# Optimization experiments

Measured on AMD Instinct MI355X. Metric: run time of the kernel, lower is better.

The kernel has to match this reference:

```python
import jax, jax.numpy as jnp
import numpy as np

B, N, D = 8, 512, 512          # batch, seq_len, n_units (== d_in for residual)
H = 8                          # n_heads
DH = D // H                    # head dim
POS_CLIP = 60
EPS = 1e-7


def setup_inputs() -> dict:
    key = jax.random.key(0)
    ks = jax.random.split(key, 16)
    s = 0.02
    inp = {
        "query": jax.random.normal(ks[0], (B, N, D), dtype=jnp.float32),
        "valid_len": jax.random.randint(ks[1], (B,), 256, N + 1, dtype=jnp.int32),
        "Wq": jax.random.normal(ks[2], (D, D), dtype=jnp.float32) * s,
        "bq": jnp.zeros((D,), jnp.float32),
        "Wk": jax.random.normal(ks[3], (D, D), dtype=jnp.float32) * s,
        "bk": jnp.zeros((D,), jnp.float32),
        "Wv": jax.random.normal(ks[4], (D, D), dtype=jnp.float32) * s,
        "bv": jnp.zeros((D,), jnp.float32),
        "Wh": jax.random.normal(ks[5], (D, D), dtype=jnp.float32) * s,
        "bh": jnp.zeros((D,), jnp.float32),
        "pos_k": jax.random.uniform(ks[6], (2 * POS_CLIP + 1, DH), dtype=jnp.float32, minval=-0.05, maxval=0.05),
        "conv1_w": jax.random.normal(ks[7], (5, 5, H, 2 * H), dtype=jnp.float32) * s,  # HWIO
        "conv1_b": jnp.zeros((2 * H,), jnp.float32),
        "norm1_gamma": jnp.ones((2 * H,), jnp.float32),
        "norm1_beta": jnp.zeros((2 * H,), jnp.float32),
        "conv2_w": jax.random.normal(ks[8], (5, 5, 2 * H, H), dtype=jnp.float32) * s,
        "conv2_b": jnp.zeros((H,), jnp.float32),
        "ln_gamma": jnp.ones((D,), jnp.float32),
        "ln_beta": jnp.zeros((D,), jnp.float32),
    }
    return inp


def _conv_same(x, k, b):
    # x: [b, n, n, cin], k: [kh, kw, cin, cout] -> [b, n, n, cout]
    y = jax.lax.conv_general_dilated(x, k, window_strides=(1, 1), padding="SAME",
                                     dimension_numbers=("NHWC", "HWIO", "NHWC"))
    return y + b


def _norm_masked(x, valid_len, gamma, beta):
    # Norm(axes=[1,2]) with tf.nn.weighted_moments; mask over the query axis (axis 1).
    b, n, m, c = x.shape
    w = (jnp.arange(n)[None, :] < valid_len[:, None]).astype(x.dtype)  # [b, n]
    w4 = w[:, :, None, None]
    sw = valid_len.astype(x.dtype)[:, None, None, None] * m            # sum of broadcast weights
    mean = jnp.sum(w4 * x, axis=(1, 2), keepdims=True) / sw
    var = jnp.sum(w4 * (x - mean) ** 2, axis=(1, 2), keepdims=True) / sw
    return gamma * (x - mean) * jax.lax.rsqrt(var + EPS) + beta


def reference(query, valid_len, Wq, bq, Wk, bk, Wv, bv, Wh, bh, pos_k,
              conv1_w, conv1_b, norm1_gamma, norm1_beta, conv2_w, conv2_b,
              ln_gamma, ln_beta):
    b, n, d_in = query.shape
    # relative position indices (Shaw et al.), clipped to +/- POS_CLIP
    rel = jnp.clip(jnp.arange(n)[None, :] - jnp.arange(n)[:, None], -POS_CLIP, POS_CLIP) + POS_CLIP
    pos_enc = pos_k[rel]                                   # [n, n, dh]

    def heads(x):
        # tf.concat(tf.split(x, H, -1), 0): head-major blocks of size b
        return x.reshape(b, n, H, DH).transpose(2, 0, 1, 3)  # [h, b, n, dh]

    q = heads(query @ Wq + bq)
    k = heads(query @ Wk + bk)
    v = heads(query @ Wv + bv)

    scores = jnp.einsum("hbnd,hbmd->hbnm", q, k) + jnp.einsum("hbnd,nmd->hbnm", q, pos_enc)
    scores = scores / jnp.sqrt(jnp.asarray(DH, scores.dtype))

    # SelfCNN over attention maps: [b, n, n, h]
    maps = scores.transpose(1, 2, 3, 0)
    y = _conv_same(maps, conv1_w, conv1_b)
    y = _norm_masked(y, valid_len, norm1_gamma, norm1_beta)
    y = jax.nn.relu(y)
    y = _conv_same(y, conv2_w, conv2_b)                    # [b, n, n, h]
    scores = y.transpose(3, 0, 1, 2)                       # [h, b, n, m]

    seq_mask = jnp.arange(n)[None, :] < valid_len[:, None]  # [b, n] over key axis
    scores = jnp.where(seq_mask[None, :, None, :], scores, jnp.asarray(-1e12, scores.dtype))
    attn = jax.nn.softmax(scores, axis=-1)

    out = jnp.einsum("hbnm,hbmd->hbnd", attn, v)
    out = out.transpose(1, 2, 0, 3).reshape(b, n, H * DH)  # merge heads back
    out = out @ Wh + bh + query                            # residual

    mean = jnp.mean(out, axis=-1, keepdims=True)
    var = jnp.var(out, axis=-1, keepdims=True)
    return ln_gamma * (out - mean) * jax.lax.rsqrt(var + EPS) + ln_beta
```

## Files before the change

kernel.cpp:

```cpp
#include <hip/hip_runtime.h>

#define PC_ 60

typedef unsigned short u16;
typedef __attribute__((ext_vector_type(8))) short short8v;
typedef __attribute__((ext_vector_type(4))) float f32x4;

__device__ inline float bf2f(u16 u) {
    union { unsigned int i; float f; } x; x.i = ((unsigned)u) << 16; return x.f;
}
__device__ inline u16 f2bf(float f) {
    union { float f; unsigned int i; } x; x.f = f;
    unsigned int r = x.i + 0x7fff + ((x.i >> 16) & 1);
    return (u16)(r >> 16);
}
__device__ inline unsigned pk2(float a, float b) {
    return (unsigned)f2bf(a) | ((unsigned)f2bf(b) << 16);
}

__global__ __launch_bounds__(256) void k_prept(
    const float* __restrict__ W0, const float* __restrict__ W1,
    const float* __restrict__ W2, const float* __restrict__ W3,
    u16* __restrict__ T0, u16* __restrict__ T1, u16* __restrict__ T2, u16* __restrict__ T3,
    const float* __restrict__ c1w, const float* __restrict__ c2w,
    const float* __restrict__ pos_k,
    u16* __restrict__ Wf1, u16* __restrict__ Wf2, u16* __restrict__ pos_kb,
    const float* __restrict__ X, u16* __restrict__ Xb)
{
    const int z = blockIdx.z;
    const int t = threadIdx.x;
    if (z == 5) {
        const int blk = blockIdx.y * 8 + blockIdx.x;
#pragma unroll
        for (int k2 = 0; k2 < 16; ++k2) {
            const int i = ((blk * 16 + k2) * 256 + t) * 8;
            float4 a = *reinterpret_cast<const float4*>(X + i);
            float4 b = *reinterpret_cast<const float4*>(X + i + 4);
            *reinterpret_cast<uint4*>(Xb + i) =
                make_uint4(pk2(a.x, a.y), pk2(a.z, a.w), pk2(b.x, b.y), pk2(b.z, b.w));
        }
        return;
    }
    if (z == 4) {
        if (blockIdx.x != 0 || blockIdx.y != 0) return;
        for (int s = t; s < 448; s += 256) {
            const int q = s >> 6, l = s & 63, lg = l >> 4, n = l & 15;
            const int G = q * 4 + lg;
            unsigned o[4];
#pragma unroll
            for (int u2 = 0; u2 < 4; ++u2) {
                float v0 = 0.f, v1 = 0.f;
                if (G < 25) {
                    const int dn = G / 5, dm = G - dn * 5;
                    v0 = c1w[((dn * 5 + dm) * 8 + u2 * 2 + 0) * 16 + n];
                    v1 = c1w[((dn * 5 + dm) * 8 + u2 * 2 + 1) * 16 + n];
                }
                o[u2] = pk2(v0, v1);
            }
            *reinterpret_cast<uint4*>(&Wf1[s * 8]) = make_uint4(o[0], o[1], o[2], o[3]);
        }
        for (int s = t; s < 832; s += 256) {
            const int q = s >> 6, l = s & 63, lg = l >> 4, n = l & 15;
            const int G = q * 4 + lg;
            unsigned o[4];
#pragma unroll
            for (int u2 = 0; u2 < 4; ++u2) {
                float v0 = 0.f, v1 = 0.f;
                if (G < 50 && n < 8) {
                    const int pos = G >> 1, h = G & 1;
                    const int dn = pos / 5, dm = pos - dn * 5;
                    v0 = c2w[((dn * 5 + dm) * 16 + h * 8 + u2 * 2 + 0) * 8 + n];
                    v1 = c2w[((dn * 5 + dm) * 16 + h * 8 + u2 * 2 + 1) * 8 + n];
                }
                o[u2] = pk2(v0, v1);
            }
            *reinterpret_cast<uint4*>(&Wf2[s * 8]) = make_uint4(o[0], o[1], o[2], o[3]);
        }
        for (int s = t; s < 128 * 64; s += 256) {
            const int r = s >> 6;
            pos_kb[s] = (r < 121) ? f2bf(pos_k[s]) : (u16)0;
        }
        return;
    }
    const float* W = (z == 0) ? W0 : (z == 1) ? W1 : (z == 2) ? W2 : W3;
    u16* T        = (z == 0) ? T0 : (z == 1) ? T1 : (z == 2) ? T2 : T3;
    __shared__ float ls[64 * 65];
    const int k0 = blockIdx.x * 64, n0 = blockIdx.y * 64;
#pragma unroll
    for (int i = 0; i < 16; ++i) {
        const int idx = t + i * 256, r = idx >> 6, c = idx & 63;
        ls[c * 65 + r] = W[(size_t)(k0 + r) * 512 + n0 + c];
    }
    __syncthreads();
#pragma unroll
    for (int i = 0; i < 16; ++i) {
        const int idx = t + i * 256, r = idx >> 6, c = idx & 63;
        T[(size_t)(n0 + r) * 512 + k0 + c] = f2bf(ls[r * 65 + c]);
    }
}

__global__ __launch_bounds__(256) void k_qkvm(
    const u16* __restrict__ Xb,
    const u16* __restrict__ WT0, const u16* __restrict__ WT1, const u16* __restrict__ WT2,
    const float* __restrict__ b0, const float* __restrict__ b1, const float* __restrict__ b2,
    u16* __restrict__ Qb, u16* __restrict__ Kb, u16* __restrict__ Vt)
{
    const int z = blockIdx.z;
    const u16* WT    = (z == 0) ? WT0 : (z == 1) ? WT1 : WT2;
    const float* bias = (z == 0) ? b0 : (z == 1) ? b1 : b2;
    __shared__ __align__(16) u16 sh[18432];
    u16* As = sh; u16* Bs = sh + 9216;
    const int t = threadIdx.x, lane = t & 63, wave = t >> 6;
    const int wm = wave >> 1, wn = wave & 1;
    const int lg = lane >> 4, ln16 = lane & 15;
    const int m0 = blockIdx.x * 128, n0 = blockIdx.y * 128;
    f32x4 acc[4][4] = {};
    for (int k0 = 0; k0 < 512; k0 += 64) {
#pragma unroll
        for (int u = 0; u < 4; ++u) {
            const int chunk = u * 256 + t, row = chunk >> 3, ko = (chunk & 7) * 8;
            *reinterpret_cast<uint4*>(As + row * 72 + ko) =
                *reinterpret_cast<const uint4*>(Xb + (size_t)(m0 + row) * 512 + k0 + ko);
            *reinterpret_cast<uint4*>(Bs + row * 72 + ko) =
                *reinterpret_cast<const uint4*>(WT + (size_t)(n0 + row) * 512 + k0 + ko);
        }
        __syncthreads();
#pragma unroll
        for (int kk = 0; kk < 64; kk += 32) {
            short8v a[4], bfr[4];
#pragma unroll
            for (int mi = 0; mi < 4; ++mi)
                a[mi] = *reinterpret_cast<const short8v*>(As + (wm * 64 + mi * 16 + ln16) * 72 + kk + lg * 8);
#pragma unroll
            for (int ni = 0; ni < 4; ++ni)
                bfr[ni] = *reinterpret_cast<const short8v*>(Bs + (wn * 64 + ni * 16 + ln16) * 72 + kk + lg * 8);
#pragma unroll
            for (int mi = 0; mi < 4; ++mi)
#pragma unroll
                for (int ni = 0; ni < 4; ++ni)
                    acc[mi][ni] = __builtin_amdgcn_mfma_f32_16x16x32_bf16(a[mi], bfr[ni], acc[mi][ni], 0, 0, 0);
        }
        __syncthreads();
    }
    u16* Cs = sh + wave * 4608;
#pragma unroll
    for (int ni = 0; ni < 4; ++ni) {
        const float bv = bias[n0 + wn * 64 + ni * 16 + ln16];
#pragma unroll
        for (int mi = 0; mi < 4; ++mi)
#pragma unroll
            for (int r = 0; r < 4; ++r)
                Cs[(mi * 16 + lg * 4 + r) * 72 + ni * 16 + ln16] = f2bf(acc[mi][ni][r] + bv);
    }
    if (z < 2) {
        u16* O = (z == 0) ? Qb : Kb;
#pragma unroll
        for (int j = 0; j < 8; ++j) {
            const int chunk = j * 64 + lane, row = chunk >> 3, co = (chunk & 7) * 8;
            const int tok = m0 + wm * 64 + row;
            const int b = tok >> 9, n = tok & 511;
            const int cg = n0 + wn * 64 + co;
            const int h = cg >> 6, dh = cg & 63;
            *reinterpret_cast<uint4*>(O + ((size_t)((b * 8 + h) * 512 + n)) * 64 + dh) =
                *reinterpret_cast<const uint4*>(Cs + row * 72 + co);
        }
    } else {
#pragma unroll
        for (int j = 0; j < 8; ++j) {
            const int chunk = j * 64 + lane, dr = chunk >> 3, no8 = (chunk & 7) * 8;
            const int cg = n0 + wn * 64 + dr;
            const int h = cg >> 6, dh = cg & 63;
            const int tok = m0 + wm * 64 + no8;
            const int b = tok >> 9, n = tok & 511;
            u16 v[8];
#pragma unroll
            for (int e = 0; e < 8; ++e) v[e] = Cs[(no8 + e) * 72 + dr];
            uint4 o = make_uint4((unsigned)v[0] | ((unsigned)v[1] << 16),
                                 (unsigned)v[2] | ((unsigned)v[3] << 16),
                                 (unsigned)v[4] | ((unsigned)v[5] << 16),
                                 (unsigned)v[6] | ((unsigned)v[7] << 16));
            *reinterpret_cast<uint4*>(Vt + ((size_t)((b * 8 + h) * 64 + dh)) * 512 + n) = o;
        }
    }
}

__global__ __launch_bounds__(256) void k_qposm(
    const u16* __restrict__ Qb, const u16* __restrict__ pos_kb, u16* __restrict__ QP)
{
    __shared__ __align__(16) u16 sh[18432];
    u16* As = sh; u16* Bs = sh + 9216;
    const int t = threadIdx.x, lane = t & 63, wave = t >> 6;
    const int lg = lane >> 4, ln16 = lane & 15;
    const int n0 = blockIdx.x * 128, bh = blockIdx.y;
#pragma unroll
    for (int u = 0; u < 4; ++u) {
        const int chunk = u * 256 + t, row = chunk >> 3, ko = (chunk & 7) * 8;
        *reinterpret_cast<uint4*>(As + row * 72 + ko) =
            *reinterpret_cast<const uint4*>(Qb + ((size_t)(bh * 512 + n0 + row)) * 64 + ko);
        *reinterpret_cast<uint4*>(Bs + row * 72 + ko) =
            *reinterpret_cast<const uint4*>(pos_kb + (size_t)row * 64 + ko);
    }
    __syncthreads();
    f32x4 acc[2][8] = {};
#pragma unroll
    for (int kk = 0; kk < 64; kk += 32) {
        short8v a[2], bfr[8];
#pragma unroll
        for (int mi = 0; mi < 2; ++mi)
            a[mi] = *reinterpret_cast<const short8v*>(As + (wave * 32 + mi * 16 + ln16) * 72 + kk + lg * 8);
#pragma unroll
        for (int ni = 0; ni < 8; ++ni)
            bfr[ni] = *reinterpret_cast<const short8v*>(Bs + (ni * 16 + ln16) * 72 + kk + lg * 8);
#pragma unroll
        for (int mi = 0; mi < 2; ++mi)
#pragma unroll
            for (int ni = 0; ni < 8; ++ni)
                acc[mi][ni] = __builtin_amdgcn_mfma_f32_16x16x32_bf16(a[mi], bfr[ni], acc[mi][ni], 0, 0, 0);
    }
    __syncthreads();
    u16* Cs = sh + wave * 4352;
#pragma unroll
    for (int mi = 0; mi < 2; ++mi)
#pragma unroll
        for (int ni = 0; ni < 8; ++ni)
#pragma unroll
            for (int r = 0; r < 4; ++r)
                Cs[(mi * 16 + lg * 4 + r) * 136 + ni * 16 + ln16] = f2bf(acc[mi][ni][r]);
#pragma unroll
    for (int j = 0; j < 8; ++j) {
        const int chunk = j * 64 + lane, row = chunk >> 4, co = (chunk & 15) * 8;
        *reinterpret_cast<uint4*>(QP + ((size_t)(bh * 512 + n0 + wave * 32 + row)) * 128 + co) =
            *reinterpret_cast<const uint4*>(Cs + row * 136 + co);
    }
}

__global__ __launch_bounds__(256) void k_scoresm(
    const u16* __restrict__ Qb, const u16* __restrict__ Kb, const u16* __restrict__ QP,
    u16* __restrict__ S)
{
    __shared__ __align__(16) u16 sh[18432];
    u16* As = sh; u16* Bs = sh + 9216;
    const int t = threadIdx.x, lane = t & 63, wave = t >> 6;
    const int wm = wave >> 1, wn = wave & 1;
    const int lg = lane >> 4, ln16 = lane & 15;
    const int bid = blockIdx.x;
    const int bb = bid & 7;
    const int rest = bid >> 3;
    const int h = rest & 7;
    const int tile = rest >> 3;
    const int mx = tile & 3, my = tile >> 2;
    const int bh = bb * 8 + h;
    const int m0 = mx * 128, n0 = my * 128;
#pragma unroll
    for (int u = 0; u < 4; ++u) {
        const int chunk = u * 256 + t, row = chunk >> 3, ko = (chunk & 7) * 8;
        *reinterpret_cast<uint4*>(As + row * 72 + ko) =
            *reinterpret_cast<const uint4*>(Qb + ((size_t)(bh * 512 + n0 + row)) * 64 + ko);
        *reinterpret_cast<uint4*>(Bs + row * 72 + ko) =
            *reinterpret_cast<const uint4*>(Kb + ((size_t)(bh * 512 + m0 + row)) * 64 + ko);
    }
    __syncthreads();
    f32x4 acc[4][4] = {};
#pragma unroll
    for (int kk = 0; kk < 64; kk += 32) {
        short8v a[4], bfr[4];
#pragma unroll
        for (int mi = 0; mi < 4; ++mi)
            a[mi] = *reinterpret_cast<const short8v*>(As + (wm * 64 + mi * 16 + ln16) * 72 + kk + lg * 8);
#pragma unroll
        for (int ni = 0; ni < 4; ++ni)
            bfr[ni] = *reinterpret_cast<const short8v*>(Bs + (wn * 64 + ni * 16 + ln16) * 72 + kk + lg * 8);
#pragma unroll
        for (int mi = 0; mi < 4; ++mi)
#pragma unroll
            for (int ni = 0; ni < 4; ++ni)
                acc[mi][ni] = __builtin_amdgcn_mfma_f32_16x16x32_bf16(a[mi], bfr[ni], acc[mi][ni], 0, 0, 0);
    }
    __syncthreads();
    u16* QPs = sh;
#pragma unroll
    for (int u = 0; u < 8; ++u) {
        const int chunk = u * 256 + t, row = chunk >> 4, co = (chunk & 15) * 8;
        *reinterpret_cast<uint4*>(QPs + row * 128 + co) =
            *reinterpret_cast<const uint4*>(QP + ((size_t)(bh * 512 + n0 + row)) * 128 + co);
    }
    __syncthreads();
#pragma unroll
    for (int mi = 0; mi < 4; ++mi)
#pragma unroll
        for (int ni = 0; ni < 4; ++ni) {
            const int m_g = m0 + wn * 64 + ni * 16 + ln16;
#pragma unroll
            for (int r = 0; r < 4; ++r) {
                const int n_loc = wm * 64 + mi * 16 + lg * 4 + r;
                const int n_g = n0 + n_loc;
                int rel = m_g - n_g;
                rel = rel < -PC_ ? -PC_ : (rel > PC_ ? PC_ : rel);
                const float v = (acc[mi][ni][r] + bf2f(QPs[n_loc * 128 + rel + PC_])) * 0.125f;
                S[(size_t)bh * 262144 + (size_t)n_g * 512 + m_g] = f2bf(v);
            }
        }
}

__global__ __launch_bounds__(256) void k_conv1m(
    const u16* __restrict__ S, const u16* __restrict__ Wf,
    const float* __restrict__ bias, u16* __restrict__ Y,
    const int* __restrict__ VL, float* __restrict__ ST)
{
    __shared__ __align__(16) u16 xs[10368];
    __shared__ float wred[4][4][8];
    const int t = threadIdx.x;
    const int bid = blockIdx.x;
    const int b = bid & 7;
    const int rest = bid >> 3;
    const int m0 = (rest & 15) * 32;
    const int n0 = (rest >> 4) * 32;
    const u16* sp0 = S + (size_t)(b * 8) * 262144;
    for (int p = t; p < 648; p += 256) {
        const int idx2 = p * 2;
        const int r = idx2 / 36, c = idx2 - r * 36;
        const int gn = n0 - 2 + r, gm = m0 - 2 + c;
        uint4 o0 = make_uint4(0, 0, 0, 0), o1 = o0;
        if ((unsigned)gn < 512u && (unsigned)gm < 512u) {
            const u16* pp = sp0 + (size_t)gn * 512 + gm;
            unsigned u[8];
#pragma unroll
            for (int e = 0; e < 8; ++e)
                u[e] = *reinterpret_cast<const unsigned*>(pp + (size_t)e * 262144);
            o0 = make_uint4((u[0] & 0xffffu) | ((u[1] & 0xffffu) << 16),
                            (u[2] & 0xffffu) | ((u[3] & 0xffffu) << 16),
                            (u[4] & 0xffffu) | ((u[5] & 0xffffu) << 16),
                            (u[6] & 0xffffu) | ((u[7] & 0xffffu) << 16));
            o1 = make_uint4((u[0] >> 16) | (u[1] & 0xffff0000u),
                            (u[2] >> 16) | (u[3] & 0xffff0000u),
                            (u[4] >> 16) | (u[5] & 0xffff0000u),
                            (u[6] >> 16) | (u[7] & 0xffff0000u));
        }
        *reinterpret_cast<uint4*>(&xs[idx2 * 8]) = o0;
        *reinterpret_cast<uint4*>(&xs[(idx2 + 1) * 8]) = o1;
    }
    const int lane = t & 63, wave = t >> 6;
    const int lg = lane >> 4, ln16 = lane & 15;
    short8v bq[7];
#pragma unroll
    for (int q = 0; q < 7; ++q)
        bq[q] = *reinterpret_cast<const short8v*>(&Wf[(q * 64 + lane) * 8]);
    int aoff[7];
#pragma unroll
    for (int q = 0; q < 7; ++q) {
        const int G = q * 4 + lg; const int p = (G < 25) ? G : 0;
        const int dn = p / 5, dm = p - dn * 5;
        aoff[q] = (dn * 36 + dm) * 8;
    }
    const float4 b4 = *reinterpret_cast<const float4*>(&bias[lg * 4]);
    const int vl = VL[b];
    f32x4 sstv = {0.f, 0.f, 0.f, 0.f}, sst2v = {0.f, 0.f, 0.f, 0.f};
    __syncthreads();
    for (int i = 0; i < 16; ++i) {
        const int j = wave * 16 + i;
        const int tr = j >> 1, c0 = (j & 1) << 4;
        const int pb = (tr * 36 + c0 + ln16) * 8;
        f32x4 acc = {b4.x, b4.y, b4.z, b4.w};
#pragma unroll
        for (int q = 0; q < 7; ++q) {
            short8v a = *reinterpret_cast<const short8v*>(&xs[pb + aoff[q]]);
            acc = __builtin_amdgcn_mfma_f32_16x16x32_bf16(bq[q], a, acc, 0, 0, 0);
        }
        u16* yb = Y + (((size_t)(b * 512 + n0 + tr)) * 512 + (m0 + c0 + ln16)) * 16 + lg * 4;
        *reinterpret_cast<uint2*>(yb) = make_uint2(pk2(acc[0], acc[1]), pk2(acc[2], acc[3]));
        if (n0 + tr < vl) {
            sstv += acc;
            sst2v += acc * acc;
        }
    }
#pragma unroll
    for (int o = 1; o < 16; o <<= 1) {
#pragma unroll
        for (int r = 0; r < 4; ++r) {
            sstv[r]  += __shfl_xor(sstv[r], o);
            sst2v[r] += __shfl_xor(sst2v[r], o);
        }
    }
    if (ln16 == 0) {
#pragma unroll
        for (int r = 0; r < 4; ++r) {
            wred[wave][lg][r]     = sstv[r];
            wred[wave][lg][4 + r] = sst2v[r];
        }
    }
    __syncthreads();
    if (t < 16) {
        const int lgg = t >> 2, r = t & 3;
        const float a  = wred[0][lgg][r] + wred[1][lgg][r] + wred[2][lgg][r] + wred[3][lgg][r];
        const float b2 = wred[0][lgg][4 + r] + wred[1][lgg][4 + r] + wred[2][lgg][4 + r] + wred[3][lgg][4 + r];
        atomicAdd(&ST[(b * 16 + t) * 2 + 0], a);
        atomicAdd(&ST[(b * 16 + t) * 2 + 1], b2);
    }
}

__global__ __launch_bounds__(256) void k_conv2m(
    const u16* __restrict__ Y, const float* __restrict__ ST,
    const int* __restrict__ VL, const float* __restrict__ n1g, const float* __restrict__ n1b,
    const u16* __restrict__ Wf, const float* __restrict__ bias,
    u16* __restrict__ S2)
{
    __shared__ __align__(16) u16 xs[20736];
    __shared__ float ssh[16][2];
    const int t = threadIdx.x;
    const int bid = blockIdx.x;
    const int b = bid & 7;
    const int rest = bid >> 3;
    const int m0 = (rest & 15) * 32;
    const int n0 = (rest >> 4) * 32;
    if (t < 16) {
        const float sw = (float)VL[b] * 512.f;
        const float mean = ST[(b * 16 + t) * 2 + 0] / sw;
        const float var  = ST[(b * 16 + t) * 2 + 1] / sw - mean * mean;
        const float sc = n1g[t] * rsqrtf(var + 1e-7f);
        ssh[t][0] = sc;
        ssh[t][1] = n1b[t] - mean * sc;
    }
    __syncthreads();
    float sc[16], shv[16];
#pragma unroll
    for (int ch = 0; ch < 16; ++ch) { sc[ch] = ssh[ch][0]; shv[ch] = ssh[ch][1]; }
    for (int idx = t; idx < 1296; idx += 256) {
        const int r = idx / 36; const int c = idx - r * 36;
        const int gn = n0 - 2 + r, gm = m0 - 2 + c;
        uint4 p0 = make_uint4(0, 0, 0, 0), p1 = p0;
        if ((unsigned)gn < 512u && (unsigned)gm < 512u) {
            const u16* yp = Y + (((size_t)(b * 512 + gn)) * 512 + gm) * 16;
            const uint4 r0 = *reinterpret_cast<const uint4*>(yp);
            const uint4 r1 = *reinterpret_cast<const uint4*>(yp + 8);
            const unsigned w0[4] = {r0.x, r0.y, r0.z, r0.w};
            const unsigned w1[4] = {r1.x, r1.y, r1.z, r1.w};
            unsigned o0[4], o1[4];
#pragma unroll
            for (int u2 = 0; u2 < 4; ++u2) {
                const int ch = u2 * 2;
                float a0 = bf2f((u16)(w0[u2] & 0xffff));
                float a1 = bf2f((u16)(w0[u2] >> 16));
                a0 = fmaf(a0, sc[ch], shv[ch]);          a0 = a0 > 0.f ? a0 : 0.f;
                a1 = fmaf(a1, sc[ch + 1], shv[ch + 1]);  a1 = a1 > 0.f ? a1 : 0.f;
                o0[u2] = pk2(a0, a1);
                const int ch2 = 8 + u2 * 2;
                float b0 = bf2f((u16)(w1[u2] & 0xffff));
                float b1 = bf2f((u16)(w1[u2] >> 16));
                b0 = fmaf(b0, sc[ch2], shv[ch2]);          b0 = b0 > 0.f ? b0 : 0.f;
                b1 = fmaf(b1, sc[ch2 + 1], shv[ch2 + 1]);  b1 = b1 > 0.f ? b1 : 0.f;
                o1[u2] = pk2(b0, b1);
            }
            p0 = make_uint4(o0[0], o0[1], o0[2], o0[3]);
            p1 = make_uint4(o1[0], o1[1], o1[2], o1[3]);
        }
        *reinterpret_cast<uint4*>(&xs[idx * 8]) = p0;
        *reinterpret_cast<uint4*>(&xs[10368 + idx * 8]) = p1;
    }
    const int lane = t & 63, wave = t >> 6;
    const int lg = lane >> 4, ln16 = lane & 15;
    short8v bq[13];
#pragma unroll
    for (int q = 0; q < 13; ++q)
        bq[q] = *reinterpret_cast<const short8v*>(&Wf[(q * 64 + lane) * 8]);
    int aoff[13];
#pragma unroll
    for (int q = 0; q < 13; ++q) {
        const int G = q * 4 + lg; const int p = (G < 50) ? G : 0;
        const int pos = p >> 1, h = p & 1;
        const int dn = pos / 5, dm = pos - dn * 5;
        aoff[q] = h * 10368 + (dn * 36 + dm) * 8;
    }
    const float bs = (ln16 < 8) ? bias[ln16] : 0.f;
    __syncthreads();
    for (int i = 0; i < 16; ++i) {
        const int j = wave * 16 + i;
        const int tr = j >> 1, c0 = (j & 1) << 4;
        const int pb = (tr * 36 + c0 + ln16) * 8;
        f32x4 acc = {bs, bs, bs, bs};
#pragma unroll
        for (int q = 0; q < 13; ++q) {
            short8v a = *reinterpret_cast<const short8v*>(&xs[pb + aoff[q]]);
            acc = __builtin_amdgcn_mfma_f32_16x16x32_bf16(a, bq[q], acc, 0, 0, 0);
        }
        if (ln16 < 8) {
            uint2 o = make_uint2(pk2(acc[0], acc[1]), pk2(acc[2], acc[3]));
            *reinterpret_cast<uint2*>(
                &S2[(((size_t)(b * 8 + ln16)) * 512 + n0 + tr) * 512 + m0 + c0 + lg * 4]) = o;
        }
    }
}

__global__ __launch_bounds__(256) void k_softav(
    const u16* __restrict__ SL, const u16* __restrict__ Vt,
    const int* __restrict__ VL, u16* __restrict__ X2)
{
    __shared__ __align__(16) u16 As[4608];
    __shared__ __align__(16) u16 Bs[4608];
    __shared__ float smx[64], siv[64];
    const int t = threadIdx.x, lane = t & 63, wave = t >> 6;
    const int lg = lane >> 4, ln16 = lane & 15;
    const int bid = blockIdx.x;
    const int b = bid & 7;
    const int rest = bid >> 3;
    const int nx = rest & 7;
    const int h = rest >> 3;
    const int n0 = nx * 64;
    const int bh = b * 8 + h;
    const int vl = VL[b];
    const u16* Sp = SL + (size_t)bh * 262144;
    for (int rr = 0; rr < 16; ++rr) {
        const int row = wave * 16 + rr;
        uint4 v = *reinterpret_cast<const uint4*>(Sp + (size_t)(n0 + row) * 512 + lane * 8);
        const unsigned w[4] = {v.x, v.y, v.z, v.w};
        float x[8];
#pragma unroll
        for (int j = 0; j < 4; ++j) {
            x[2 * j]     = bf2f((u16)(w[j] & 0xffff));
            x[2 * j + 1] = bf2f((u16)(w[j] >> 16));
        }
        const int mb = lane * 8;
        float mx = -3.0e38f;
#pragma unroll
        for (int j = 0; j < 8; ++j) {
            if (mb + j >= vl) x[j] = -3.0e38f;
            mx = fmaxf(mx, x[j]);
        }
#pragma unroll
        for (int o = 32; o; o >>= 1) mx = fmaxf(mx, __shfl_xor(mx, o));
        float sm = 0.f;
#pragma unroll
        for (int j = 0; j < 8; ++j) sm += __expf(x[j] - mx);
#pragma unroll
        for (int o = 32; o; o >>= 1) sm += __shfl_xor(sm, o);
        if (lane == 0) { smx[row] = mx; siv[row] = 1.0f / sm; }
    }
    __syncthreads();
    f32x4 acc[4] = {};
    for (int k0 = 0; k0 < 512; k0 += 64) {
#pragma unroll
        for (int u = 0; u < 2; ++u) {
            const int chunk = u * 256 + t, row = chunk >> 3, ko = (chunk & 7) * 8;
            uint4 raw = *reinterpret_cast<const uint4*>(Sp + (size_t)(n0 + row) * 512 + k0 + ko);
            const unsigned w[4] = {raw.x, raw.y, raw.z, raw.w};
            const float mxr = smx[row], ivr = siv[row];
            unsigned o[4];
#pragma unroll
            for (int jj = 0; jj < 4; ++jj) {
                const int m0i = k0 + ko + 2 * jj;
                float a0 = (m0i     < vl) ? __expf(bf2f((u16)(w[jj] & 0xffff)) - mxr) * ivr : 0.f;
                float a1 = (m0i + 1 < vl) ? __expf(bf2f((u16)(w[jj] >> 16))   - mxr) * ivr : 0.f;
                o[jj] = pk2(a0, a1);
            }
            *reinterpret_cast<uint4*>(As + row * 72 + ko) = make_uint4(o[0], o[1], o[2], o[3]);
            *reinterpret_cast<uint4*>(Bs + row * 72 + ko) =
                *reinterpret_cast<const uint4*>(Vt + ((size_t)(bh * 64 + row)) * 512 + k0 + ko);
        }
        __syncthreads();
#pragma unroll
        for (int kk = 0; kk < 64; kk += 32) {
            short8v a = *reinterpret_cast<const short8v*>(As + (wave * 16 + ln16) * 72 + kk + lg * 8);
#pragma unroll
            for (int ni = 0; ni < 4; ++ni) {
                short8v bfr = *reinterpret_cast<const short8v*>(Bs + (ni * 16 + ln16) * 72 + kk + lg * 8);
                acc[ni] = __builtin_amdgcn_mfma_f32_16x16x32_bf16(a, bfr, acc[ni], 0, 0, 0);
            }
        }
        __syncthreads();
    }
    u16* Cs = As + wave * 1152;
#pragma unroll
    for (int ni = 0; ni < 4; ++ni)
#pragma unroll
        for (int r = 0; r < 4; ++r)
            Cs[(lg * 4 + r) * 72 + ni * 16 + ln16] = f2bf(acc[ni][r]);
#pragma unroll
    for (int j = 0; j < 2; ++j) {
        const int chunk = j * 64 + lane, row = chunk >> 3, co = (chunk & 7) * 8;
        const int tn = n0 + wave * 16 + row;
        *reinterpret_cast<uint4*>(X2 + ((size_t)(b * 512 + tn)) * 512 + h * 64 + co) =
            *reinterpret_cast<const uint4*>(Cs + row * 72 + co);
    }
}

__global__ __launch_bounds__(256) void k_outm(
    const u16* __restrict__ X2, const u16* __restrict__ WT, const float* __restrict__ bias,
    const float* __restrict__ Xq, float* __restrict__ Pout)
{
    __shared__ __align__(16) u16 sh[18432];
    u16* As = sh; u16* Bs = sh + 9216;
    const int t = threadIdx.x, lane = t & 63, wave = t >> 6;
    const int wm = wave >> 1, wn = wave & 1;
    const int lg = lane >> 4, ln16 = lane & 15;
    const int m0 = blockIdx.x * 128, n0 = blockIdx.y * 128;
    f32x4 acc[4][4] = {};
    for (int k0 = 0; k0 < 512; k0 += 64) {
#pragma unroll
        for (int u = 0; u < 4; ++u) {
            const int chunk = u * 256 + t, row = chunk >> 3, ko = (chunk & 7) * 8;
            *reinterpret_cast<uint4*>(As + row * 72 + ko) =
                *reinterpret_cast<const uint4*>(X2 + (size_t)(m0 + row) * 512 + k0 + ko);
            *reinterpret_cast<uint4*>(Bs + row * 72 + ko) =
                *reinterpret_cast<const uint4*>(WT + (size_t)(n0 + row) * 512 + k0 + ko);
        }
        __syncthreads();
#pragma unroll
        for (int kk = 0; kk < 64; kk += 32) {
            short8v a[4], bfr[4];
#pragma unroll
            for (int mi = 0; mi < 4; ++mi)
                a[mi] = *reinterpret_cast<const short8v*>(As + (wm * 64 + mi * 16 + ln16) * 72 + kk + lg * 8);
#pragma unroll
            for (int ni = 0; ni < 4; ++ni)
                bfr[ni] = *reinterpret_cast<const short8v*>(Bs + (wn * 64 + ni * 16 + ln16) * 72 + kk + lg * 8);
#pragma unroll
            for (int mi = 0; mi < 4; ++mi)
#pragma unroll
                for (int ni = 0; ni < 4; ++ni)
                    acc[mi][ni] = __builtin_amdgcn_mfma_f32_16x16x32_bf16(a[mi], bfr[ni], acc[mi][ni], 0, 0, 0);
        }
        __syncthreads();
    }
#pragma unroll
    for (int ni = 0; ni < 4; ++ni) {
        const int cg = n0 + wn * 64 + ni * 16 + ln16;
        const float bv = bias[cg];
#pragma unroll
        for (int mi = 0; mi < 4; ++mi)
#pragma unroll
            for (int r = 0; r < 4; ++r) {
                const int tok = m0 + wm * 64 + mi * 16 + lg * 4 + r;
                Pout[(size_t)tok * 512 + cg] = acc[mi][ni][r] + bv + Xq[(size_t)tok * 512 + cg];
            }
    }
}

__global__ __launch_bounds__(256) void k_ln(
    const float* __restrict__ P, const float* __restrict__ g,
    const float* __restrict__ be, float* __restrict__ out)
{
    const int row = blockIdx.x * 4 + (threadIdx.x >> 6);
    const int lane = threadIdx.x & 63;
    const float* p = P + (size_t)row * 512;
    float4 v0 = reinterpret_cast<const float4*>(p)[lane];
    float4 v1 = reinterpret_cast<const float4*>(p)[64 + lane];
    float s = v0.x + v0.y + v0.z + v0.w + v1.x + v1.y + v1.z + v1.w;
#pragma unroll
    for (int o = 32; o; o >>= 1) s += __shfl_xor(s, o);
    const float mean = s * (1.0f / 512.0f);
    float d[8] = {v0.x - mean, v0.y - mean, v0.z - mean, v0.w - mean,
                  v1.x - mean, v1.y - mean, v1.z - mean, v1.w - mean};
    float s2 = 0.f;
#pragma unroll
    for (int j = 0; j < 8; ++j) s2 += d[j] * d[j];
#pragma unroll
    for (int o = 32; o; o >>= 1) s2 += __shfl_xor(s2, o);
    const float rstd = rsqrtf(s2 * (1.0f / 512.0f) + 1e-7f);
    float4 g0 = reinterpret_cast<const float4*>(g)[lane];
    float4 g1 = reinterpret_cast<const float4*>(g)[64 + lane];
    float4 b0 = reinterpret_cast<const float4*>(be)[lane];
    float4 b1 = reinterpret_cast<const float4*>(be)[64 + lane];
    float* op = out + (size_t)row * 512;
    reinterpret_cast<float4*>(op)[lane] =
        make_float4(d[0] * rstd * g0.x + b0.x, d[1] * rstd * g0.y + b0.y,
                    d[2] * rstd * g0.z + b0.z, d[3] * rstd * g0.w + b0.w);
    reinterpret_cast<float4*>(op)[64 + lane] =
        make_float4(d[4] * rstd * g1.x + b1.x, d[5] * rstd * g1.y + b1.y,
                    d[6] * rstd * g1.z + b1.z, d[7] * rstd * g1.w + b1.w);
}

extern "C" void kernel_launch(void* const* d_in, const int* in_sizes, int n_in,
                              void* d_out, int out_size, void* d_ws, size_t ws_size,
                              hipStream_t stream)
{
    const float* query = (const float*)d_in[0];
    const int*   VL    = (const int*)d_in[1];
    const float* Wq = (const float*)d_in[2];  const float* bq = (const float*)d_in[3];
    const float* Wk = (const float*)d_in[4];  const float* bk = (const float*)d_in[5];
    const float* Wv = (const float*)d_in[6];  const float* bv = (const float*)d_in[7];
    const float* Wh = (const float*)d_in[8];  const float* bh = (const float*)d_in[9];
    const float* pos_k = (const float*)d_in[10];
    const float* c1w = (const float*)d_in[11]; const float* c1b = (const float*)d_in[12];
    const float* n1g = (const float*)d_in[13]; const float* n1b = (const float*)d_in[14];
    const float* c2w = (const float*)d_in[15]; const float* c2b = (const float*)d_in[16];
    const float* lng = (const float*)d_in[17]; const float* lnb = (const float*)d_in[18];

    float* ws = (float*)d_ws;
    const size_t M1 = (size_t)1 << 20;
    u16* S1  = (u16*)ws;
    u16* Y1  = (u16*)(ws + 8 * M1);
    u16* Xb  = (u16*)(ws + 24 * M1);
    u16* Qb  = (u16*)(ws + 25 * M1);
    u16* Kb  = (u16*)(ws + 26 * M1);
    u16* Vt  = (u16*)(ws + 27 * M1);
    u16* QPb = (u16*)(ws + 28 * M1);
    u16* WqT = (u16*)(ws + 30 * M1);
    u16* WkT = WqT + 262144;
    u16* WvT = WkT + 262144;
    u16* WhT = WvT + 262144;
    u16* pos_kb = (u16*)(ws + 30 * M1 + 524288);
    u16* Wf1 = pos_kb + 8192;
    u16* Wf2 = Wf1 + 3584;
    float* ST  = ws + 31 * M1;
    u16* X2 = Xb;
    float* Pout = ws + 28 * M1;

    hipMemsetAsync(ST, 0, 256 * sizeof(float), stream);

    k_prept<<<dim3(8, 8, 6), 256, 0, stream>>>(Wq, Wk, Wv, Wh, WqT, WkT, WvT, WhT,
                                               c1w, c2w, pos_k, Wf1, Wf2, pos_kb,
                                               query, Xb);
    k_qkvm<<<dim3(32, 4, 3), 256, 0, stream>>>(Xb, WqT, WkT, WvT, bq, bk, bv, Qb, Kb, Vt);
    k_qposm<<<dim3(4, 64), 256, 0, stream>>>(Qb, pos_kb, QPb);
    k_scoresm<<<1024, 256, 0, stream>>>(Qb, Kb, QPb, S1);
    k_conv1m<<<2048, 256, 0, stream>>>(S1, Wf1, c1b, Y1, VL, ST);
    k_conv2m<<<2048, 256, 0, stream>>>(Y1, ST, VL, n1g, n1b, Wf2, c2b, S1);
    k_softav<<<512, 256, 0, stream>>>(S1, Vt, VL, X2);
    k_outm<<<dim3(32, 4), 256, 0, stream>>>(X2, WhT, bh, query, Pout);
    k_ln<<<1024, 256, 0, stream>>>(Pout, lng, lnb, (float*)d_out);
}
```

Baseline: 256.3 us.

## Fuse softmax partial stats into conv2 and vectorize score stores

```diff
diff --git a/kernel.cpp b/kernel.cpp
--- a/kernel.cpp
+++ b/kernel.cpp
@@ -274,32 +274,35 @@
         for (int mi = 0; mi < 4; ++mi)
 #pragma unroll
             for (int ni = 0; ni < 4; ++ni)
-                acc[mi][ni] = __builtin_amdgcn_mfma_f32_16x16x32_bf16(a[mi], bfr[ni], acc[mi][ni], 0, 0, 0);
+                acc[mi][ni] = __builtin_amdgcn_mfma_f32_16x16x32_bf16(bfr[ni], a[mi], acc[mi][ni], 0, 0, 0);
     }
     __syncthreads();
     u16* QPs = sh;
 #pragma unroll
     for (int u = 0; u < 8; ++u) {
         const int chunk = u * 256 + t, row = chunk >> 4, co = (chunk & 15) * 8;
-        *reinterpret_cast<uint4*>(QPs + row * 128 + co) =
+        *reinterpret_cast<uint4*>(QPs + row * 136 + co) =
             *reinterpret_cast<const uint4*>(QP + ((size_t)(bh * 512 + n0 + row)) * 128 + co);
     }
     __syncthreads();
 #pragma unroll
-    for (int mi = 0; mi < 4; ++mi)
+    for (int mi = 0; mi < 4; ++mi) {
+        const int n_loc = wm * 64 + mi * 16 + ln16;
+        const int n_g = n0 + n_loc;
 #pragma unroll
         for (int ni = 0; ni < 4; ++ni) {
-            const int m_g = m0 + wn * 64 + ni * 16 + ln16;
+            const int mb = m0 + wn * 64 + ni * 16 + lg * 4;
+            float v[4];
 #pragma unroll
             for (int r = 0; r < 4; ++r) {
-                const int n_loc = wm * 64 + mi * 16 + lg * 4 + r;
-                const int n_g = n0 + n_loc;
-                int rel = m_g - n_g;
+                int rel = (mb + r) - n_g;
                 rel = rel < -PC_ ? -PC_ : (rel > PC_ ? PC_ : rel);
-                const float v = (acc[mi][ni][r] + bf2f(QPs[n_loc * 128 + rel + PC_])) * 0.125f;
-                S[(size_t)bh * 262144 + (size_t)n_g * 512 + m_g] = f2bf(v);
-            }
-        }
+                v[r] = (acc[mi][ni][r] + bf2f(QPs[n_loc * 136 + rel + PC_])) * 0.125f;
+            }
+            *reinterpret_cast<uint2*>(&S[(size_t)bh * 262144 + (size_t)n_g * 512 + mb]) =
+                make_uint2(pk2(v[0], v[1]), pk2(v[2], v[3]));
+        }
+    }
 }
 
 __global__ __launch_bounds__(256) void k_conv1m(
@@ -402,7 +405,7 @@
     const u16* __restrict__ Y, const float* __restrict__ ST,
     const int* __restrict__ VL, const float* __restrict__ n1g, const float* __restrict__ n1b,
     const u16* __restrict__ Wf, const float* __restrict__ bias,
-    u16* __restrict__ S2)
+    u16* __restrict__ S2, float2* __restrict__ PS)
 {
     __shared__ __align__(16) u16 xs[20736];
     __shared__ float ssh[16][2];
@@ -412,8 +415,9 @@
     const int rest = bid >> 3;
     const int m0 = (rest & 15) * 32;
     const int n0 = (rest >> 4) * 32;
+    const int vl = VL[b];
     if (t < 16) {
-        const float sw = (float)VL[b] * 512.f;
+        const float sw = (float)vl * 512.f;
         const float mean = ST[(b * 16 + t) * 2 + 0] / sw;
         const float var  = ST[(b * 16 + t) * 2 + 1] / sw - mean * mean;
         const float sc = n1g[t] * rsqrtf(var + 1e-7f);
@@ -472,27 +476,51 @@
     }
     const float bs = (ln16 < 8) ? bias[ln16] : 0.f;
     __syncthreads();
-    for (int i = 0; i < 16; ++i) {
-        const int j = wave * 16 + i;
-        const int tr = j >> 1, c0 = (j & 1) << 4;
-        const int pb = (tr * 36 + c0 + ln16) * 8;
-        f32x4 acc = {bs, bs, bs, bs};
-#pragma unroll
-        for (int q = 0; q < 13; ++q) {
-            short8v a = *reinterpret_cast<const short8v*>(&xs[pb + aoff[q]]);
-            acc = __builtin_amdgcn_mfma_f32_16x16x32_bf16(a, bq[q], acc, 0, 0, 0);
-        }
-        if (ln16 < 8) {
-            uint2 o = make_uint2(pk2(acc[0], acc[1]), pk2(acc[2], acc[3]));
-            *reinterpret_cast<uint2*>(
-                &S2[(((size_t)(b * 8 + ln16)) * 512 + n0 + tr) * 512 + m0 + c0 + lg * 4]) = o;
-        }
+    for (int ip = 0; ip < 8; ++ip) {
+        const int tr = wave * 8 + ip;
+        float xv[8];
+#pragma unroll
+        for (int half = 0; half < 2; ++half) {
+            const int c0 = half << 4;
+            const int pb = (tr * 36 + c0 + ln16) * 8;
+            f32x4 acc = {bs, bs, bs, bs};
+#pragma unroll
+            for (int q = 0; q < 13; ++q) {
+                short8v a = *reinterpret_cast<const short8v*>(&xs[pb + aoff[q]]);
+                acc = __builtin_amdgcn_mfma_f32_16x16x32_bf16(a, bq[q], acc, 0, 0, 0);
+            }
+            if (ln16 < 8) {
+                uint2 o = make_uint2(pk2(acc[0], acc[1]), pk2(acc[2], acc[3]));
+                *reinterpret_cast<uint2*>(
+                    &S2[(((size_t)(b * 8 + ln16)) * 512 + n0 + tr) * 512 + m0 + c0 + lg * 4]) = o;
+            }
+#pragma unroll
+            for (int r = 0; r < 4; ++r) {
+                const int m = m0 + c0 + lg * 4 + r;
+                xv[half * 4 + r] = (m < vl) ? acc[r] : -3.0e38f;
+            }
+        }
+        float mxr = xv[0];
+#pragma unroll
+        for (int r8 = 1; r8 < 8; ++r8) mxr = fmaxf(mxr, xv[r8]);
+        mxr = fmaxf(mxr, __shfl_xor(mxr, 16));
+        mxr = fmaxf(mxr, __shfl_xor(mxr, 32));
+        float smr = 0.f;
+#pragma unroll
+        for (int r8 = 0; r8 < 8; ++r8) {
+            const int m = m0 + ((r8 >> 2) << 4) + lg * 4 + (r8 & 3);
+            smr += (m < vl) ? __expf(xv[r8] - mxr) : 0.f;
+        }
+        smr += __shfl_xor(smr, 16);
+        smr += __shfl_xor(smr, 32);
+        if (lg == 0 && ln16 < 8)
+            PS[((size_t)(b * 8 + ln16) * 512 + n0 + tr) * 16 + (m0 >> 5)] = make_float2(mxr, smr);
     }
 }
 
 __global__ __launch_bounds__(256) void k_softav(
     const u16* __restrict__ SL, const u16* __restrict__ Vt,
-    const int* __restrict__ VL, u16* __restrict__ X2)
+    const int* __restrict__ VL, const float2* __restrict__ PS, u16* __restrict__ X2)
 {
     __shared__ __align__(16) u16 As[4608];
     __shared__ __align__(16) u16 Bs[4608];
@@ -508,31 +536,22 @@
     const int bh = b * 8 + h;
     const int vl = VL[b];
     const u16* Sp = SL + (size_t)bh * 262144;
-    for (int rr = 0; rr < 16; ++rr) {
-        const int row = wave * 16 + rr;
-        uint4 v = *reinterpret_cast<const uint4*>(Sp + (size_t)(n0 + row) * 512 + lane * 8);
-        const unsigned w[4] = {v.x, v.y, v.z, v.w};
-        float x[8];
-#pragma unroll
-        for (int j = 0; j < 4; ++j) {
-            x[2 * j]     = bf2f((u16)(w[j] & 0xffff));
-            x[2 * j + 1] = bf2f((u16)(w[j] >> 16));
-        }
-        const int mb = lane * 8;
-        float mx = -3.0e38f;
-#pragma unroll
-        for (int j = 0; j < 8; ++j) {
-            if (mb + j >= vl) x[j] = -3.0e38f;
-            mx = fmaxf(mx, x[j]);
-        }
-#pragma unroll
-        for (int o = 32; o; o >>= 1) mx = fmaxf(mx, __shfl_xor(mx, o));
-        float sm = 0.f;
-#pragma unroll
-        for (int j = 0; j < 8; ++j) sm += __expf(x[j] - mx);
-#pragma unroll
-        for (int o = 32; o; o >>= 1) sm += __shfl_xor(sm, o);
-        if (lane == 0) { smx[row] = mx; siv[row] = 1.0f / sm; }
+    if (t < 64) {
+        const float* pp = reinterpret_cast<const float*>(PS) + ((size_t)bh * 512 + n0 + t) * 32;
+        float mxv[16], smv[16];
+#pragma unroll
+        for (int i = 0; i < 8; ++i) {
+            float4 v = *reinterpret_cast<const float4*>(pp + i * 4);
+            mxv[i * 2]     = v.x; smv[i * 2]     = v.y;
+            mxv[i * 2 + 1] = v.z; smv[i * 2 + 1] = v.w;
+        }
+        float M = mxv[0];
+#pragma unroll
+        for (int i = 1; i < 16; ++i) M = fmaxf(M, mxv[i]);
+        float Ssum = 0.f;
+#pragma unroll
+        for (int i = 0; i < 16; ++i) Ssum += smv[i] * __expf(mxv[i] - M);
+        smx[t] = M; siv[t] = 1.0f / Ssum;
     }
     __syncthreads();
     f32x4 acc[4] = {};
@@ -701,6 +720,7 @@
     u16* Wf1 = pos_kb + 8192;
     u16* Wf2 = Wf1 + 3584;
     float* ST  = ws + 31 * M1;
+    float2* PS = (float2*)(ws + 31 * M1 + 512);
     u16* X2 = Xb;
     float* Pout = ws + 28 * M1;
 
@@ -713,8 +733,8 @@
     k_qposm<<<dim3(4, 64), 256, 0, stream>>>(Qb, pos_kb, QPb);
     k_scoresm<<<1024, 256, 0, stream>>>(Qb, Kb, QPb, S1);
     k_conv1m<<<2048, 256, 0, stream>>>(S1, Wf1, c1b, Y1, VL, ST);
-    k_conv2m<<<2048, 256, 0, stream>>>(Y1, ST, VL, n1g, n1b, Wf2, c2b, S1);
-    k_softav<<<512, 256, 0, stream>>>(S1, Vt, VL, X2);
+    k_conv2m<<<2048, 256, 0, stream>>>(Y1, ST, VL, n1g, n1b, Wf2, c2b, S1, PS);
+    k_softav<<<512, 256, 0, stream>>>(S1, Vt, VL, PS, X2);
     k_outm<<<dim3(32, 4), 256, 0, stream>>>(X2, WhT, bh, query, Pout);
     k_ln<<<1024, 256, 0, stream>>>(Pout, lng, lnb, (float*)d_out);
 }
```

After: 255.3 us. Within noise of the previous version (-0.4%).
